# Optimization experiments

Measured on AMD Instinct MI355X. Metric: run time of the kernel, lower is better.

## Reference

```python
import jax, jax.numpy as jnp
import numpy as np
from jax import lax

CR = 16        # opt.cr (temporal dim)
HEADS = 4      # num_heads
DIM = 64       # dim == channel count c
B = 2          # true batch; input batch = B*CR
H = W = 128


def setup_inputs() -> dict:
    key = jax.random.key(0)
    k1, k2, k3, k4 = jax.random.split(key, 4)
    return {
        "x": jax.random.normal(k1, (B * CR, DIM, H, W), jnp.float32),
        "ln_weight": jnp.ones((DIM,), jnp.float32),
        "ln_bias": jnp.zeros((DIM,), jnp.float32),
        "qkv_w": jax.random.normal(k2, (3 * CR, CR), jnp.float32) * 0.05,   # 1x1 conv
        "dw_w": jax.random.normal(k3, (3 * CR, 1, 3, 3), jnp.float32) * 0.1,  # depthwise 3x3
        "proj_w": jax.random.normal(k4, (DIM, DIM), jnp.float32) * 0.05,   # 1x1 conv
        "temperature": jnp.ones((HEADS, 1, 1), jnp.float32),
    }


def reference(x, ln_weight, ln_bias, qkv_w, dw_w, proj_w, temperature):
    b, c, h, w = x.shape
    Bt = b // CR
    # WithBias LayerNorm over channel dim (per spatial location), eps=1e-5
    mu = jnp.mean(x, axis=1, keepdims=True)
    var = jnp.mean(jnp.square(x - mu), axis=1, keepdims=True)
    xn = (x - mu) / jnp.sqrt(var + 1e-5)
    xn = xn * ln_weight[None, :, None, None] + ln_bias[None, :, None, None]
    # (B*cr, c, h, w) -> (B, cr, c, h, w) -> (B*c, cr, h, w)
    x_in = xn.reshape(Bt, CR, c, h, w).transpose(0, 2, 1, 3, 4).reshape(Bt * c, CR, h, w)
    # 1x1 qkv conv (no bias)
    qkv = jnp.einsum('oc,bchw->bohw', qkv_w, x_in)
    # depthwise 3x3 conv, padding 1
    qkv = lax.conv_general_dilated(qkv, dw_w, (1, 1), 'SAME',
                                   feature_group_count=3 * CR,
                                   dimension_numbers=('NCHW', 'OIHW', 'NCHW'))
    q, k, v = jnp.split(qkv, 3, axis=1)
    ch = CR // HEADS  # per-head channel dim

    def heads(t):
        return t.reshape(Bt * c, HEADS, ch, h * w)

    def l2n(t):
        n = jnp.sqrt(jnp.sum(jnp.square(t), axis=-1, keepdims=True))
        return t / jnp.maximum(n, 1e-12)

    q, k, v = heads(q), heads(k), heads(v)
    q, k = l2n(q), l2n(k)
    # transposed (channel) attention: small ch x ch scores
    attn = jnp.einsum('bhcn,bhdn->bhcd', q, k) * temperature[None]
    attn = jax.nn.softmax(attn, axis=-1)
    out = jnp.einsum('bhcd,bhdn->bhcn', attn, v)  # (B*c, heads, ch, hw)
    # (B*c, cr, h, w) -> (B, c, cr, h, w) -> (B*cr, c, h, w)
    out = out.reshape(Bt * c, CR, h, w).reshape(Bt, c, CR, h, w)
    out = out.transpose(0, 2, 1, 3, 4).reshape(b, c, h, w)
    # 1x1 project_out
    return jnp.einsum('oc,bchw->bohw', proj_w, out)
```

## Files before the change

kernel.cpp:

```cpp
#include <hip/hip_runtime.h>
#include <hip/hip_fp16.h>

typedef _Float16 half8_t __attribute__((ext_vector_type(8)));
typedef float float4_t __attribute__((ext_vector_type(4)));

__device__ __forceinline__ float2 h2f2(unsigned int u) {
  return __half22float2(__builtin_bit_cast(__half2, u));
}
__device__ __forceinline__ unsigned int f2h2(float a, float b) {
  return __builtin_bit_cast(unsigned int, __floats2half2_rn(a, b));
}

#if __has_builtin(__builtin_amdgcn_fdot2)
typedef _Float16 h2v __attribute__((ext_vector_type(2)));
__device__ __forceinline__ float fdot2(unsigned int a, unsigned int b, float c) {
  return __builtin_amdgcn_fdot2(__builtin_bit_cast(h2v, a),
                                __builtin_bit_cast(h2v, b), c, false);
}
#else
__device__ __forceinline__ float fdot2(unsigned int a, unsigned int b, float c) {
  float2 fa = h2f2(a), fb = h2f2(b);
  return fmaf(fa.y, fb.y, fmaf(fa.x, fb.x, c));
}
#endif

__global__ __launch_bounds__(256) void k_statsxn(
    const float2* __restrict__ x2, const float* __restrict__ lnw,
    const float* __restrict__ lnb, unsigned int* __restrict__ xnw,
    const float* __restrict__ qkvw, const float* __restrict__ dww,
    const float* __restrict__ projw, unsigned int* __restrict__ qkvpk,
    unsigned int* __restrict__ dwpk, unsigned int* __restrict__ projpk) {
  int bt = blockIdx.y;
  if (blockIdx.x >= 512) {
    if (bt == 0) {
      for (int t = threadIdx.x; t < 2648; t += 256) {
        if (t < 2048) {
          int o = t >> 5, c2 = t & 31;
          projpk[t] = f2h2(projw[(o << 6) + 2 * c2], projw[(o << 6) + 2 * c2 + 1]);
        } else if (t < 2432) {
          int i = t - 2048;
          int ch = i >> 3, tp = i & 7;
          qkvpk[i] = f2h2(qkvw[(ch << 4) + 2 * tp], qkvw[(ch << 4) + 2 * tp + 1]);
        } else {
          int i = t - 2432;
          int pl = i / 9, k = i - pl * 9;
          dwpk[i] = f2h2(dww[18 * pl + k], dww[18 * pl + 9 + k]);
        }
      }
    }
    return;
  }
  int tid = threadIdx.x;
  int t = tid >> 4, j = tid & 15;
  int jp = (blockIdx.x << 4) + j;
  int bb = (bt << 4) + t;
  const float2* xp = x2 + ((size_t)bb << 19) + jp;
  float s0 = 0.f, q0 = 0.f, s1 = 0.f, q1 = 0.f;
#pragma unroll 8
  for (int ci = 0; ci < 64; ++ci) {
    float2 v = xp[(size_t)ci << 13];
    s0 += v.x; q0 = fmaf(v.x, v.x, q0);
    s1 += v.y; q1 = fmaf(v.y, v.y, q1);
  }
  float mu0 = s0 * (1.f / 64.f), mu1 = s1 * (1.f / 64.f);
  float r0 = rsqrtf(fmaf(-mu0, mu0, q0 * (1.f / 64.f)) + 1e-5f);
  float r1 = rsqrtf(fmaf(-mu1, mu1, q1 * (1.f / 64.f)) + 1e-5f);
  asm volatile("" ::: "memory");
  int px = (jp << 1) + (t & 1);
  size_t obase = (size_t)px * 8 + (t >> 1);
#pragma unroll 8
  for (int ci = 0; ci < 64; ++ci) {
    float2 v = xp[(size_t)ci << 13];
    float lw = lnw[ci], lb = lnb[ci];
    unsigned int u = f2h2(fmaf((v.x - mu0) * r0, lw, lb),
                          fmaf((v.y - mu1) * r1, lw, lb));
    unsigned int pu = __shfl_xor(u, 16);
    unsigned int w = (!(t & 1)) ? ((u & 0xFFFFu) | (pu << 16))
                                : ((pu >> 16) | (u & 0xFFFF0000u));
    xnw[((size_t)((bt << 6) + ci) << 17) + obase] = w;
  }
}

__global__ __launch_bounds__(256) void k_fused(
    const unsigned int* __restrict__ xnw, const unsigned int* __restrict__ qkvpk,
    const unsigned int* __restrict__ dwpk, unsigned int* __restrict__ vbuf,
    float* __restrict__ Sacc, float* __restrict__ Nacc) {
  __shared__ unsigned int pre[3232];
  __shared__ unsigned int qk[2080];
  int tid = threadIdx.x;
  int bc = blockIdx.y;
  int tx0 = (blockIdx.x & 3) << 5;
  int ty0 = (blockIdx.x >> 2) << 3;
  int lane15 = tid & 15;
  int kg = (tid >> 4) & 3;
  int wv = tid >> 6;
  int jx = tid & 7, iy = (tid >> 3) & 7;

  uint4 bfr[6];
  int pwa[6];
#pragma unroll
  for (int i = 0; i < 6; ++i) {
    int T = wv + 4 * i;
    int hp = T * 16 + lane15;
    int hy = hp / 36, hx = hp - hy * 36;
    int gy = ty0 + hy - 1, gx = tx0 + hx - 2;
    bool val = hp < 360;
    bool ok = val && ((unsigned)gy < 128u) && ((unsigned)gx < 128u);
    pwa[i] = val ? (hy * 40 + hx) : -1;
    uint4 bw = make_uint4(0, 0, 0, 0);
    if (ok && kg < 2)
      bw = *reinterpret_cast<const uint4*>(
          &xnw[((size_t)bc << 17) + (size_t)((gy << 7) + gx) * 8 + 4 * kg]);
    bfr[i] = bw;
  }

  for (int m = 0; m < 3; ++m) {
    if (m > 0) {
      int pm = m - 1;
      {
        int combo = tid >> 3, pc = tid & 7;
        int hp_ = combo >> 4, cd = combo & 15, cc = cd >> 2, dd = cd & 3;
        const unsigned int* qrow = qk + (4 * hp_ + cc) * 130;
        const unsigned int* krow = qk + (8 + 4 * hp_ + dd) * 130;
        float s = 0.f;
#pragma unroll
        for (int i = 0; i < 8; ++i) {
          uint2 q2 = *reinterpret_cast<const uint2*>(&qrow[2 * pc + (i << 4)]);
          uint2 k2 = *reinterpret_cast<const uint2*>(&krow[2 * pc + (i << 4)]);
          s = fdot2(q2.x, k2.x, s);
          s = fdot2(q2.y, k2.y, s);
        }
        s += __shfl_xor(s, 1); s += __shfl_xor(s, 2); s += __shfl_xor(s, 4);
        if (pc == 0)
          atomicAdd(&Sacc[((bc << 2) + 2 * pm + hp_) * 16 + cc * 4 + dd], s);
      }
      {
        int row = tid >> 4, pc = tid & 15;
        const unsigned int* rp = qk + row * 130;
        float n = 0.f;
#pragma unroll
        for (int i = 0; i < 4; ++i) {
          uint2 v2 = *reinterpret_cast<const uint2*>(&rp[2 * pc + (i << 5)]);
          n = fdot2(v2.x, v2.x, n);
          n = fdot2(v2.y, v2.y, n);
        }
        n += __shfl_xor(n, 1); n += __shfl_xor(n, 2);
        n += __shfl_xor(n, 4); n += __shfl_xor(n, 8);
        if (pc == 0) {
          int g = (row < 8) ? (8 * pm + row) : (16 + 8 * pm + (row - 8));
          atomicAdd(&Nacc[(bc << 5) + g], n);
        }
      }
    }
    {
      int gch = (m < 2)
                    ? ((lane15 < 8) ? (8 * m + lane15) : (16 + 8 * m + (lane15 - 8)))
                    : (32 + lane15);
      uint4 aw = make_uint4(0, 0, 0, 0);
      if (kg < 2) aw = *reinterpret_cast<const uint4*>(&qkvpk[gch * 8 + 4 * kg]);
      half8_t af = __builtin_bit_cast(half8_t, aw);
      float4_t zz = {0.f, 0.f, 0.f, 0.f};
#pragma unroll
      for (int i = 0; i < 6; ++i) {
        half8_t bf = __builtin_bit_cast(half8_t, bfr[i]);
        float4_t d = __builtin_amdgcn_mfma_f32_16x16x32_f16(af, bf, zz, 0, 0, 0);
        if (pwa[i] >= 0) {
          pre[(2 * kg) * 404 + pwa[i]] = f2h2(d[0], d[1]);
          pre[(2 * kg + 1) * 404 + pwa[i]] = f2h2(d[2], d[3]);
        }
      }
    }
    __syncthreads();
#pragma unroll
    for (int p2 = 0; p2 < 2; ++p2) {
      int pl = wv + 4 * p2;
      int gpl = (m < 2) ? ((pl < 4) ? (4 * m + pl) : (8 + 4 * m + (pl - 4)))
                        : (16 + pl);
      const unsigned int* wp = dwpk + gpl * 9;
      __half2 a0 = __floats2half2_rn(0.f, 0.f), a1 = a0, a2 = a0, a3 = a0;
      int base = pl * 404 + iy * 40 + 4 * jx;
#pragma unroll
      for (int dy = 0; dy < 3; ++dy) {
        uint4 C0 = *reinterpret_cast<const uint4*>(&pre[base + dy * 40]);
        uint4 C1 = *reinterpret_cast<const uint4*>(&pre[base + dy * 40 + 4]);
        __half2 c1 = __builtin_bit_cast(__half2, C0.y);
        __half2 c2 = __builtin_bit_cast(__half2, C0.z);
        __half2 c3 = __builtin_bit_cast(__half2, C0.w);
        __half2 c4 = __builtin_bit_cast(__half2, C1.x);
        __half2 c5 = __builtin_bit_cast(__half2, C1.y);
        __half2 c6 = __builtin_bit_cast(__half2, C1.z);
        __half2 w0 = __builtin_bit_cast(__half2, wp[dy * 3 + 0]);
        __half2 w1 = __builtin_bit_cast(__half2, wp[dy * 3 + 1]);
        __half2 w2 = __builtin_bit_cast(__half2, wp[dy * 3 + 2]);
        a0 = __hfma2(w0, c1, a0); a0 = __hfma2(w1, c2, a0); a0 = __hfma2(w2, c3, a0);
        a1 = __hfma2(w0, c2, a1); a1 = __hfma2(w1, c3, a1); a1 = __hfma2(w2, c4, a1);
        a2 = __hfma2(w0, c3, a2); a2 = __hfma2(w1, c4, a2); a2 = __hfma2(w2, c5, a2);
        a3 = __hfma2(w0, c4, a3); a3 = __hfma2(w1, c5, a3); a3 = __hfma2(w2, c6, a3);
      }
      unsigned int u0 = __builtin_bit_cast(unsigned int, a0);
      unsigned int u1 = __builtin_bit_cast(unsigned int, a1);
      unsigned int u2 = __builtin_bit_cast(unsigned int, a2);
      unsigned int u3 = __builtin_bit_cast(unsigned int, a3);
      if (m < 2) {
        uint2 E, O;
        E.x = (u0 & 0xFFFFu) | (u1 << 16);
        E.y = (u2 & 0xFFFFu) | (u3 << 16);
        O.x = (u0 >> 16) | (u1 & 0xFFFF0000u);
        O.y = (u2 >> 16) | (u3 & 0xFFFF0000u);
        int pp = iy * 16 + 2 * jx;
        *reinterpret_cast<uint2*>(&qk[(2 * pl) * 130 + pp]) = E;
        *reinterpret_cast<uint2*>(&qk[(2 * pl + 1) * 130 + pp]) = O;
      } else {
        size_t idx = ((size_t)(bc * 8 + pl) << 14) +
                     (size_t)((ty0 + iy) << 7) + tx0 + 4 * jx;
        *reinterpret_cast<uint4*>(&vbuf[idx]) = make_uint4(u0, u1, u2, u3);
      }
    }
    if (m < 2) __syncthreads();
  }
}

__global__ __launch_bounds__(256) void k_outproj(
    const unsigned int* __restrict__ vbuf, const float* __restrict__ Sacc,
    const float* __restrict__ Nacc, const float* __restrict__ temp,
    const unsigned int* __restrict__ projpk, float* __restrict__ out) {
  __shared__ unsigned int Yl[32 * 260];
  __shared__ unsigned int attn_l[128];
  int tid = threadIdx.x;
  int comb = blockIdx.y;
  int bt = comb >> 4, hd = (comb >> 2) & 3, c = comb & 3;
  int lane15 = tid & 15;
  int kg = (tid >> 4) & 3;
  int wv = tid >> 6;

  if (tid < 64) {
    int b = (bt << 6) + tid;
    float tp = temp[hd];
    float iq = 1.f / fmaxf(sqrtf(Nacc[(b << 5) + (hd << 2) + c]), 1e-12f);
    float l[4];
#pragma unroll
    for (int d = 0; d < 4; ++d) {
      float ik = 1.f / fmaxf(sqrtf(Nacc[(b << 5) + 16 + (hd << 2) + d]), 1e-12f);
      l[d] = Sacc[((b << 2) + hd) * 16 + c * 4 + d] * iq * ik * tp;
    }
    float mx = fmaxf(fmaxf(l[0], l[1]), fmaxf(l[2], l[3]));
    float e0 = expf(l[0] - mx), e1 = expf(l[1] - mx);
    float e2 = expf(l[2] - mx), e3 = expf(l[3] - mx);
    float inv = 1.f / (e0 + e1 + e2 + e3);
    attn_l[2 * tid] = f2h2(e0 * inv, e1 * inv);
    attn_l[2 * tid + 1] = f2h2(e2 * inv, e3 * inv);
  }
  __syncthreads();

  {
    int gpx = (blockIdx.x << 8) + tid;
    size_t vb = (((size_t)bt * 512 + hd * 2) << 14) + gpx;
#pragma unroll
    for (int ci2 = 0; ci2 < 32; ++ci2) {
      size_t b0 = vb + (((size_t)(2 * ci2) * 8) << 14);
      size_t b1 = b0 + ((size_t)8 << 14);
      unsigned int va0 = vbuf[b0], vb0 = vbuf[b0 + 16384];
      unsigned int va1 = vbuf[b1], vb1 = vbuf[b1 + 16384];
      uint4 aw = *reinterpret_cast<const uint4*>(&attn_l[4 * ci2]);
      float y0 = fdot2(va0, aw.x, fdot2(vb0, aw.y, 0.f));
      float y1 = fdot2(va1, aw.z, fdot2(vb1, aw.w, 0.f));
      Yl[ci2 * 260 + tid] = f2h2(y0, y1);
    }
  }
  __syncthreads();

  half8_t A0[4], A1[4];
#pragma unroll
  for (int ot = 0; ot < 4; ++ot) {
    A0[ot] = __builtin_bit_cast(
        half8_t, *reinterpret_cast<const uint4*>(
                     &projpk[(ot * 16 + lane15) * 32 + kg * 4]));
    A1[ot] = __builtin_bit_cast(
        half8_t, *reinterpret_cast<const uint4*>(
                     &projpk[(ot * 16 + lane15) * 32 + 16 + kg * 4]));
  }
  float4_t zz = {0.f, 0.f, 0.f, 0.f};
  size_t outbase = ((size_t)comb << 20) + (blockIdx.x << 8);
#pragma unroll
  for (int pt = 0; pt < 4; ++pt) {
    int pxl = wv * 64 + pt * 16 + lane15;
    unsigned int r0 = Yl[(kg * 4 + 0) * 260 + pxl];
    unsigned int r1 = Yl[(kg * 4 + 1) * 260 + pxl];
    unsigned int r2 = Yl[(kg * 4 + 2) * 260 + pxl];
    unsigned int r3 = Yl[(kg * 4 + 3) * 260 + pxl];
    half8_t B0 = __builtin_bit_cast(half8_t, make_uint4(r0, r1, r2, r3));
    unsigned int s0 = Yl[(16 + kg * 4 + 0) * 260 + pxl];
    unsigned int s1 = Yl[(16 + kg * 4 + 1) * 260 + pxl];
    unsigned int s2 = Yl[(16 + kg * 4 + 2) * 260 + pxl];
    unsigned int s3 = Yl[(16 + kg * 4 + 3) * 260 + pxl];
    half8_t B1 = __builtin_bit_cast(half8_t, make_uint4(s0, s1, s2, s3));
#pragma unroll
    for (int ot = 0; ot < 4; ++ot) {
      float4_t d = __builtin_amdgcn_mfma_f32_16x16x32_f16(A0[ot], B0, zz, 0, 0, 0);
      d = __builtin_amdgcn_mfma_f32_16x16x32_f16(A1[ot], B1, d, 0, 0, 0);
      int o0 = ot * 16 + kg * 4;
#pragma unroll
      for (int r = 0; r < 4; ++r)
        out[outbase + ((size_t)(o0 + r) << 14) + pxl] = d[r];
    }
  }
}

extern "C" void kernel_launch(void* const* d_in, const int* in_sizes, int n_in,
                              void* d_out, int out_size, void* d_ws, size_t ws_size,
                              hipStream_t stream) {
  const float* x = (const float*)d_in[0];
  const float* lnw = (const float*)d_in[1];
  const float* lnb = (const float*)d_in[2];
  const float* qkvw = (const float*)d_in[3];
  const float* dww = (const float*)d_in[4];
  const float* projw = (const float*)d_in[5];
  const float* temp = (const float*)d_in[6];
  float* out = (float*)d_out;

  unsigned int* xnw = (unsigned int*)d_ws;
  unsigned int* vbuf = xnw + (67108864ull / 4);
  char* tail = (char*)d_ws + 134217728ull;
  float* Sacc = (float*)tail;
  float* Nacc = Sacc + 8192;
  unsigned int* projpk = (unsigned int*)(Nacc + 4096);
  unsigned int* qkvpk = projpk + 2048;
  unsigned int* dwpk = qkvpk + 384;

  hipMemsetAsync(Sacc, 0, (8192 + 4096) * sizeof(float), stream);
  k_statsxn<<<dim3(513, 2), dim3(256), 0, stream>>>(
      (const float2*)x, lnw, lnb, xnw, qkvw, dww, projw, qkvpk, dwpk, projpk);
  k_fused<<<dim3(64, 128), dim3(256), 0, stream>>>(xnw, qkvpk, dwpk, vbuf, Sacc,
                                                   Nacc);
  k_outproj<<<dim3(64, 32), dim3(256), 0, stream>>>(vbuf, Sacc, Nacc, temp,
                                                    projpk, out);
}
```

Before: 212.5 us.

## Split LayerNorm into stats and normalize kernels; interleave V buffer planes

```diff
diff --git a/kernel.cpp b/kernel.cpp
--- a/kernel.cpp
+++ b/kernel.cpp
@@ -24,61 +24,71 @@
 }
 #endif
 
-__global__ __launch_bounds__(256) void k_statsxn(
-    const float2* __restrict__ x2, const float* __restrict__ lnw,
-    const float* __restrict__ lnb, unsigned int* __restrict__ xnw,
+__global__ __launch_bounds__(256) void k_stats(
+    const float2* __restrict__ x2, float4* __restrict__ stats4,
     const float* __restrict__ qkvw, const float* __restrict__ dww,
     const float* __restrict__ projw, unsigned int* __restrict__ qkvpk,
     unsigned int* __restrict__ dwpk, unsigned int* __restrict__ projpk) {
-  int bt = blockIdx.y;
-  if (blockIdx.x >= 512) {
-    if (bt == 0) {
-      for (int t = threadIdx.x; t < 2648; t += 256) {
-        if (t < 2048) {
-          int o = t >> 5, c2 = t & 31;
-          projpk[t] = f2h2(projw[(o << 6) + 2 * c2], projw[(o << 6) + 2 * c2 + 1]);
-        } else if (t < 2432) {
-          int i = t - 2048;
-          int ch = i >> 3, tp = i & 7;
-          qkvpk[i] = f2h2(qkvw[(ch << 4) + 2 * tp], qkvw[(ch << 4) + 2 * tp + 1]);
-        } else {
-          int i = t - 2432;
-          int pl = i / 9, k = i - pl * 9;
-          dwpk[i] = f2h2(dww[18 * pl + k], dww[18 * pl + 9 + k]);
-        }
+  if (blockIdx.x >= 1024) {
+    for (int t = threadIdx.x; t < 2648; t += 256) {
+      if (t < 2048) {
+        int o = t >> 5, c2 = t & 31;
+        projpk[t] = f2h2(projw[(o << 6) + 2 * c2], projw[(o << 6) + 2 * c2 + 1]);
+      } else if (t < 2432) {
+        int i = t - 2048;
+        int ch = i >> 3, tp = i & 7;
+        qkvpk[i] = f2h2(qkvw[(ch << 4) + 2 * tp], qkvw[(ch << 4) + 2 * tp + 1]);
+      } else {
+        int i = t - 2432;
+        int pl = i / 9, k = i - pl * 9;
+        dwpk[i] = f2h2(dww[18 * pl + k], dww[18 * pl + 9 + k]);
       }
     }
     return;
   }
-  int tid = threadIdx.x;
-  int t = tid >> 4, j = tid & 15;
-  int jp = (blockIdx.x << 4) + j;
-  int bb = (bt << 4) + t;
+  int id = blockIdx.x * 256 + threadIdx.x;
+  int bb = id >> 13;
+  int jp = id & 8191;
   const float2* xp = x2 + ((size_t)bb << 19) + jp;
   float s0 = 0.f, q0 = 0.f, s1 = 0.f, q1 = 0.f;
-#pragma unroll 8
+#pragma unroll
   for (int ci = 0; ci < 64; ++ci) {
     float2 v = xp[(size_t)ci << 13];
     s0 += v.x; q0 = fmaf(v.x, v.x, q0);
     s1 += v.y; q1 = fmaf(v.y, v.y, q1);
   }
   float mu0 = s0 * (1.f / 64.f), mu1 = s1 * (1.f / 64.f);
-  float r0 = rsqrtf(fmaf(-mu0, mu0, q0 * (1.f / 64.f)) + 1e-5f);
-  float r1 = rsqrtf(fmaf(-mu1, mu1, q1 * (1.f / 64.f)) + 1e-5f);
-  asm volatile("" ::: "memory");
-  int px = (jp << 1) + (t & 1);
-  size_t obase = (size_t)px * 8 + (t >> 1);
-#pragma unroll 8
-  for (int ci = 0; ci < 64; ++ci) {
-    float2 v = xp[(size_t)ci << 13];
-    float lw = lnw[ci], lb = lnb[ci];
-    unsigned int u = f2h2(fmaf((v.x - mu0) * r0, lw, lb),
-                          fmaf((v.y - mu1) * r1, lw, lb));
-    unsigned int pu = __shfl_xor(u, 16);
-    unsigned int w = (!(t & 1)) ? ((u & 0xFFFFu) | (pu << 16))
-                                : ((pu >> 16) | (u & 0xFFFF0000u));
-    xnw[((size_t)((bt << 6) + ci) << 17) + obase] = w;
-  }
+  float4 r;
+  r.x = mu0; r.y = rsqrtf(fmaf(-mu0, mu0, q0 * (1.f / 64.f)) + 1e-5f);
+  r.z = mu1; r.w = rsqrtf(fmaf(-mu1, mu1, q1 * (1.f / 64.f)) + 1e-5f);
+  stats4[id] = r;
+}
+
+__global__ __launch_bounds__(256) void k_xn(
+    const float2* __restrict__ x2, const float4* __restrict__ stats4,
+    const float* __restrict__ lnw, const float* __restrict__ lnb,
+    unsigned int* __restrict__ xnw) {
+  int bc = blockIdx.y, bt = bc >> 6, ci = bc & 63;
+  int jp = blockIdx.x * 256 + threadIdx.x;
+  float lw = lnw[ci], lb = lnb[ci];
+  unsigned int w0[8], w1[8];
+#pragma unroll
+  for (int tp = 0; tp < 8; ++tp) {
+    int bb0 = (bt << 4) + 2 * tp;
+    float2 xa = x2[(((size_t)((bb0 << 6) + ci)) << 13) + jp];
+    float2 xb = x2[(((size_t)(((bb0 + 1) << 6) + ci)) << 13) + jp];
+    float4 sa = stats4[((size_t)bb0 << 13) + jp];
+    float4 sb = stats4[((size_t)(bb0 + 1) << 13) + jp];
+    w0[tp] = f2h2(fmaf((xa.x - sa.x) * sa.y, lw, lb),
+                  fmaf((xb.x - sb.x) * sb.y, lw, lb));
+    w1[tp] = f2h2(fmaf((xa.y - sa.z) * sa.w, lw, lb),
+                  fmaf((xb.y - sb.z) * sb.w, lw, lb));
+  }
+  size_t base = (((size_t)bc << 14) + 2 * (size_t)jp) * 8;
+  *reinterpret_cast<uint4*>(&xnw[base + 0]) = make_uint4(w0[0], w0[1], w0[2], w0[3]);
+  *reinterpret_cast<uint4*>(&xnw[base + 4]) = make_uint4(w0[4], w0[5], w0[6], w0[7]);
+  *reinterpret_cast<uint4*>(&xnw[base + 8]) = make_uint4(w1[0], w1[1], w1[2], w1[3]);
+  *reinterpret_cast<uint4*>(&xnw[base + 12]) = make_uint4(w1[4], w1[5], w1[6], w1[7]);
 }
 
 __global__ __launch_bounds__(256) void k_fused(
@@ -171,9 +181,10 @@
       }
     }
     __syncthreads();
+    unsigned int vs[2][4];
 #pragma unroll
     for (int p2 = 0; p2 < 2; ++p2) {
-      int pl = wv + 4 * p2;
+      int pl = 2 * wv + p2;
       int gpl = (m < 2) ? ((pl < 4) ? (4 * m + pl) : (8 + 4 * m + (pl - 4)))
                         : (16 + pl);
       const unsigned int* wp = dwpk + gpl * 9;
@@ -211,12 +222,19 @@
         *reinterpret_cast<uint2*>(&qk[(2 * pl) * 130 + pp]) = E;
         *reinterpret_cast<uint2*>(&qk[(2 * pl + 1) * 130 + pp]) = O;
       } else {
-        size_t idx = ((size_t)(bc * 8 + pl) << 14) +
-                     (size_t)((ty0 + iy) << 7) + tx0 + 4 * jx;
-        *reinterpret_cast<uint4*>(&vbuf[idx]) = make_uint4(u0, u1, u2, u3);
-      }
-    }
-    if (m < 2) __syncthreads();
+        vs[p2][0] = u0; vs[p2][1] = u1; vs[p2][2] = u2; vs[p2][3] = u3;
+      }
+    }
+    if (m == 2) {
+      size_t vb2 = (((size_t)(bc * 4 + wv)) << 15) +
+                   (size_t)(((ty0 + iy) << 7) + tx0 + 4 * jx) * 2;
+      *reinterpret_cast<uint4*>(&vbuf[vb2]) =
+          make_uint4(vs[0][0], vs[1][0], vs[0][1], vs[1][1]);
+      *reinterpret_cast<uint4*>(&vbuf[vb2 + 4]) =
+          make_uint4(vs[0][2], vs[1][2], vs[0][3], vs[1][3]);
+    } else {
+      __syncthreads();
+    }
   }
 }
 
@@ -254,16 +272,14 @@
 
   {
     int gpx = (blockIdx.x << 8) + tid;
-    size_t vb = (((size_t)bt * 512 + hd * 2) << 14) + gpx;
+    size_t vb = (((size_t)(bt * 256 + hd)) << 15) + (size_t)gpx * 2;
 #pragma unroll
     for (int ci2 = 0; ci2 < 32; ++ci2) {
-      size_t b0 = vb + (((size_t)(2 * ci2) * 8) << 14);
-      size_t b1 = b0 + ((size_t)8 << 14);
-      unsigned int va0 = vbuf[b0], vb0 = vbuf[b0 + 16384];
-      unsigned int va1 = vbuf[b1], vb1 = vbuf[b1 + 16384];
+      uint2 A0 = *reinterpret_cast<const uint2*>(&vbuf[vb + ((size_t)(2 * ci2) << 17)]);
+      uint2 A1 = *reinterpret_cast<const uint2*>(&vbuf[vb + ((size_t)(2 * ci2 + 1) << 17)]);
       uint4 aw = *reinterpret_cast<const uint4*>(&attn_l[4 * ci2]);
-      float y0 = fdot2(va0, aw.x, fdot2(vb0, aw.y, 0.f));
-      float y1 = fdot2(va1, aw.z, fdot2(vb1, aw.w, 0.f));
+      float y0 = fdot2(A0.x, aw.x, fdot2(A0.y, aw.y, 0.f));
+      float y1 = fdot2(A1.x, aw.z, fdot2(A1.y, aw.w, 0.f));
       Yl[ci2 * 260 + tid] = f2h2(y0, y1);
     }
   }
@@ -321,15 +337,18 @@
   unsigned int* xnw = (unsigned int*)d_ws;
   unsigned int* vbuf = xnw + (67108864ull / 4);
   char* tail = (char*)d_ws + 134217728ull;
-  float* Sacc = (float*)tail;
+  float4* stats4 = (float4*)tail;
+  float* Sacc = (float*)(tail + 4194304ull);
   float* Nacc = Sacc + 8192;
   unsigned int* projpk = (unsigned int*)(Nacc + 4096);
   unsigned int* qkvpk = projpk + 2048;
   unsigned int* dwpk = qkvpk + 384;
 
   hipMemsetAsync(Sacc, 0, (8192 + 4096) * sizeof(float), stream);
-  k_statsxn<<<dim3(513, 2), dim3(256), 0, stream>>>(
-      (const float2*)x, lnw, lnb, xnw, qkvw, dww, projw, qkvpk, dwpk, projpk);
+  k_stats<<<dim3(1025), dim3(256), 0, stream>>>((const float2*)x, stats4, qkvw,
+                                                dww, projw, qkvpk, dwpk, projpk);
+  k_xn<<<dim3(32, 128), dim3(256), 0, stream>>>((const float2*)x, stats4, lnw,
+                                                lnb, xnw);
   k_fused<<<dim3(64, 128), dim3(256), 0, stream>>>(xnw, qkvpk, dwpk, vbuf, Sacc,
                                                    Nacc);
   k_outproj<<<dim3(64, 32), dim3(256), 0, stream>>>(vbuf, Sacc, Nacc, temp,
```

Result: slower. 223.4 us (+5.1%).
